# Kernel optimization log

Hardware: AMD Instinct MI355X
Metric: run time of the kernel (lower is better)

The kernel has to match this reference:

```python
import jax, jax.numpy as jnp
import numpy as np

Q_MAX = 127.0  # 8-bit, narrow range [-127, 127] (pytorch-quantization default)


def fake_quant(x, amax):
    """Fake quantization with clipped-STE semantics (matches pytorch-quantization).

    amax may be a scalar (per-tensor) or broadcastable (per-channel). Treated as
    a constant (stop_gradient'd by caller where appropriate).
    """
    amax = jnp.maximum(amax, 1e-12)
    scale = amax / Q_MAX
    xq = jnp.round(jnp.clip(x / scale, -Q_MAX, Q_MAX)) * scale
    xc = jnp.clip(x, -amax, amax)  # identity grad inside range, zero outside
    return xc + jax.lax.stop_gradient(xq - xc)


def quant_conv1x1(x, w, b):
    """QuantConv2d with 1x1 kernel: fake-quant input (per-tensor dynamic max amax)
    and weight (per-output-channel max amax), then conv + bias.
    x: [B,C,H,W], w: [O,C], b: [O]
    """
    a_amax = jax.lax.stop_gradient(jnp.max(jnp.abs(x)))
    xq = fake_quant(x, a_amax)
    w_amax = jax.lax.stop_gradient(jnp.max(jnp.abs(w), axis=1, keepdims=True))
    wq = fake_quant(w, w_amax)
    y = jnp.einsum('bchw,oc->bohw', xq, wq)
    return y + b[None, :, None, None]


def setup_inputs() -> dict:
    key = jax.random.key(0)
    k1, k2, k3, k4 = jax.random.split(key, 4)
    B, C, Cr, H, W = 64, 32, 8, 128, 128
    x = jax.random.normal(k1, (B, C, H, W), dtype=jnp.float32)
    identity = jax.random.normal(k2, (B, C, H, W), dtype=jnp.float32)
    w_reduce = jax.random.normal(k3, (Cr, C), dtype=jnp.float32) * 0.1
    b_reduce = jnp.zeros((Cr,), dtype=jnp.float32)
    w_expand = jax.random.normal(k4, (C, Cr), dtype=jnp.float32) * 0.1
    b_expand = jnp.zeros((C,), dtype=jnp.float32)
    return {"x": x, "identity": identity,
            "w_reduce": w_reduce, "b_reduce": b_reduce,
            "w_expand": w_expand, "b_expand": b_expand}


def reference(x, identity, w_reduce, b_reduce, w_expand, b_expand):
    h = quant_conv1x1(x, w_reduce, b_reduce)      # [B,8,H,W]
    h = h * jax.nn.sigmoid(h)                     # SiLU
    g = quant_conv1x1(h, w_expand, b_expand)      # [B,32,H,W]
    return identity * jax.nn.sigmoid(g)
```

## Files before the change

kernel.cpp:

```cpp
#include <hip/hip_runtime.h>
#include <math.h>

#define QMAX 127.0f
#define CIN 32
#define CR 8
#define HW 16384
#define BATCH 64
#define NPIX (BATCH*HW)
#define NQUAD (NPIX/4)
#define NX (BATCH*CIN*HW)

#define H_OFF 64
#define WS_NEEDED ((size_t)(H_OFF + (size_t)NPIX * CR) * 4)

__device__ __forceinline__ float fq(float v, float inv_scale, float scale) {
    return rintf(fminf(fmaxf(v * inv_scale, -QMAX), QMAX)) * scale;
}
__device__ __forceinline__ float sigmoidf_(float v) {
    return 1.0f / (1.0f + __expf(-v));
}

__global__ __launch_bounds__(256) void k1_xmax(const float4* __restrict__ x4,
                                               unsigned int* __restrict__ wsu) {
    int idx = blockIdx.x * 256 + threadIdx.x;
    float m = 0.f;
#pragma unroll
    for (int i = 0; i < 16; i++) {
        float4 v = x4[idx + i * 524288];
        m = fmaxf(m, fmaxf(fmaxf(fabsf(v.x), fabsf(v.y)), fmaxf(fabsf(v.z), fabsf(v.w))));
    }
#pragma unroll
    for (int off = 32; off > 0; off >>= 1) m = fmaxf(m, __shfl_xor(m, off, 64));
    __shared__ float red[4];
    int t = threadIdx.x;
    if ((t & 63) == 0) red[t >> 6] = m;
    __syncthreads();
    if (t == 0) {
        m = fmaxf(fmaxf(red[0], red[1]), fmaxf(red[2], red[3]));
        atomicMax(&wsu[0], __float_as_uint(m));
    }
}

__global__ __launch_bounds__(256) void k2_hmax(const float* __restrict__ x,
                                               const float* __restrict__ wr,
                                               const float* __restrict__ br,
                                               const unsigned int* __restrict__ wsu,
                                               unsigned int* __restrict__ hmax,
                                               float* __restrict__ hbuf) {
    __shared__ float wq[CR * CIN], bsh[CR], amr[CR];
    int t = threadIdx.x;
    if (t < CR) {
        float mm = 0.f;
        for (int c = 0; c < CIN; c++) mm = fmaxf(mm, fabsf(wr[t * CIN + c]));
        amr[t] = fmaxf(mm, 1e-12f);
        bsh[t] = br[t];
    }
    __syncthreads();
    {
        float amax = amr[t >> 5];
        wq[t] = fq(wr[t], QMAX / amax, amax * (1.f / QMAX));
    }
    __syncthreads();
    float a_amax = fmaxf(__uint_as_float(wsu[0]), 1e-12f);
    float scale = a_amax * (1.f / QMAX), inv_scale = QMAX / a_amax;
    int tid = blockIdx.x * 256 + t;
    int b = tid >> 12;
    int hw = (tid & 4095) << 2;
    const float* xb = x + (size_t)b * CIN * HW + hw;
    float hacc[CR][4];
#pragma unroll
    for (int o = 0; o < CR; o++)
#pragma unroll
        for (int v = 0; v < 4; v++) hacc[o][v] = 0.f;
#pragma unroll
    for (int c = 0; c < CIN; c++) {
        float4 xv = *(const float4*)(xb + (size_t)c * HW);
        float q0 = fq(xv.x, inv_scale, scale), q1 = fq(xv.y, inv_scale, scale);
        float q2 = fq(xv.z, inv_scale, scale), q3 = fq(xv.w, inv_scale, scale);
#pragma unroll
        for (int o = 0; o < CR; o++) {
            float w = wq[o * CIN + c];
            hacc[o][0] += q0 * w; hacc[o][1] += q1 * w;
            hacc[o][2] += q2 * w; hacc[o][3] += q3 * w;
        }
    }
    float m = 0.f;
#pragma unroll
    for (int o = 0; o < CR; o++) {
        float bb = bsh[o];
        float4 hv;
        float* hp = (float*)&hv;
#pragma unroll
        for (int v = 0; v < 4; v++) {
            float h = hacc[o][v] + bb;
            h = h * sigmoidf_(h);
            hp[v] = h;
            m = fmaxf(m, fabsf(h));
        }
        if (hbuf) *(float4*)(hbuf + ((size_t)(b * CR + o)) * HW + hw) = hv;
    }
#pragma unroll
    for (int off = 32; off > 0; off >>= 1) m = fmaxf(m, __shfl_xor(m, off, 64));
    __shared__ float red[4];
    if ((t & 63) == 0) red[t >> 6] = m;
    __syncthreads();
    if (t == 0) {
        m = fmaxf(fmaxf(red[0], red[1]), fmaxf(red[2], red[3]));
        atomicMax(hmax, __float_as_uint(m));
    }
}

__global__ __launch_bounds__(256) void k3_out(const float* __restrict__ hbuf,
                                              const float* __restrict__ identity,
                                              const float* __restrict__ we,
                                              const float* __restrict__ be,
                                              const unsigned int* __restrict__ wsu,
                                              float* __restrict__ out) {
    const int y = blockIdx.y;
    __shared__ float wqe[16 * CR], besh[16], ame[16];
    int t = threadIdx.x;
    if (t < 16) {
        int r = 16 * y + t;
        float mm = 0.f;
        for (int c = 0; c < CR; c++) mm = fmaxf(mm, fabsf(we[r * CR + c]));
        ame[t] = fmaxf(mm, 1e-12f);
        besh[t] = be[r];
    }
    __syncthreads();
    if (t < 128) {
        int r16 = t >> 3;
        float amax = ame[r16];
        wqe[t] = fq(we[(16 * y + r16) * CR + (t & 7)], QMAX / amax, amax * (1.f / QMAX));
    }
    __syncthreads();
    float h_amax = fmaxf(__uint_as_float(wsu[1]), 1e-12f);
    float hscale = h_amax * (1.f / QMAX), hinv = QMAX / h_amax;
    int tid = blockIdx.x * 256 + t;
    int b = tid >> 12;
    int hw = (tid & 4095) << 2;
    size_t base = (size_t)b * CIN * HW + hw;

    float hq[CR][4];
#pragma unroll
    for (int cr = 0; cr < CR; cr++) {
        float4 hv = *(const float4*)(hbuf + ((size_t)(b * CR + cr)) * HW + hw);
        hq[cr][0] = fq(hv.x, hinv, hscale);
        hq[cr][1] = fq(hv.y, hinv, hscale);
        hq[cr][2] = fq(hv.z, hinv, hscale);
        hq[cr][3] = fq(hv.w, hinv, hscale);
    }
#pragma unroll 4
    for (int o = 0; o < 16; o++) {
        float g0 = besh[o], g1 = g0, g2 = g0, g3 = g0;
#pragma unroll
        for (int cr = 0; cr < CR; cr++) {
            float w = wqe[o * CR + cr];
            g0 += hq[cr][0] * w; g1 += hq[cr][1] * w;
            g2 += hq[cr][2] * w; g3 += hq[cr][3] * w;
        }
        size_t off = base + (size_t)(16 * y + o) * HW;
        float4 idv = *(const float4*)(identity + off);
        float4 ov;
        ov.x = idv.x * sigmoidf_(g0);
        ov.y = idv.y * sigmoidf_(g1);
        ov.z = idv.z * sigmoidf_(g2);
        ov.w = idv.w * sigmoidf_(g3);
        *(float4*)(out + off) = ov;
    }
}

__global__ __launch_bounds__(256) void k3_out_rc(const float* __restrict__ x,
                                                 const float* __restrict__ identity,
                                                 const float* __restrict__ wr,
                                                 const float* __restrict__ br,
                                                 const float* __restrict__ we,
                                                 const float* __restrict__ be,
                                                 const unsigned int* __restrict__ wsu,
                                                 float* __restrict__ out) {
    __shared__ float wqr[CR * CIN], wqe[CIN * CR], bsh[CR], besh[CIN], amr[CR], ame[CIN];
    int t = threadIdx.x;
    if (t < CR) {
        float mm = 0.f;
        for (int c = 0; c < CIN; c++) mm = fmaxf(mm, fabsf(wr[t * CIN + c]));
        amr[t] = fmaxf(mm, 1e-12f);
        bsh[t] = br[t];
    }
    if (t >= 64 && t < 64 + CIN) {
        int r = t - 64;
        float mm = 0.f;
        for (int c = 0; c < CR; c++) mm = fmaxf(mm, fabsf(we[r * CR + c]));
        ame[r] = fmaxf(mm, 1e-12f);
        besh[r] = be[r];
    }
    __syncthreads();
    {
        float amax = amr[t >> 5];
        wqr[t] = fq(wr[t], QMAX / amax, amax * (1.f / QMAX));
        float amax2 = ame[t >> 3];
        wqe[t] = fq(we[t], QMAX / amax2, amax2 * (1.f / QMAX));
    }
    __syncthreads();
    float a_amax = fmaxf(__uint_as_float(wsu[0]), 1e-12f);
    float ascale = a_amax * (1.f / QMAX), ainv = QMAX / a_amax;
    float h_amax = fmaxf(__uint_as_float(wsu[1]), 1e-12f);
    float hscale = h_amax * (1.f / QMAX), hinv = QMAX / h_amax;
    int tid = blockIdx.x * 256 + t;
    int b = tid >> 12;
    int hw = (tid & 4095) << 2;
    size_t base = (size_t)b * CIN * HW + hw;
    const float* xb = x + base;
    float hq[CR][4];
    {
        float hacc[CR][4];
#pragma unroll
        for (int o = 0; o < CR; o++)
#pragma unroll
            for (int v = 0; v < 4; v++) hacc[o][v] = 0.f;
#pragma unroll
        for (int c = 0; c < CIN; c++) {
            float4 xv = *(const float4*)(xb + (size_t)c * HW);
            float q0 = fq(xv.x, ainv, ascale), q1 = fq(xv.y, ainv, ascale);
            float q2 = fq(xv.z, ainv, ascale), q3 = fq(xv.w, ainv, ascale);
#pragma unroll
            for (int o = 0; o < CR; o++) {
                float w = wqr[o * CIN + c];
                hacc[o][0] += q0 * w; hacc[o][1] += q1 * w;
                hacc[o][2] += q2 * w; hacc[o][3] += q3 * w;
            }
        }
#pragma unroll
        for (int o = 0; o < CR; o++) {
            float bb = bsh[o];
#pragma unroll
            for (int v = 0; v < 4; v++) {
                float h = hacc[o][v] + bb;
                h = h * sigmoidf_(h);
                hq[o][v] = fq(h, hinv, hscale);
            }
        }
    }
#pragma unroll 4
    for (int o2 = 0; o2 < CIN; o2++) {
        float g0 = besh[o2], g1 = g0, g2 = g0, g3 = g0;
#pragma unroll
        for (int cr = 0; cr < CR; cr++) {
            float w = wqe[o2 * CR + cr];
            g0 += hq[cr][0] * w; g1 += hq[cr][1] * w;
            g2 += hq[cr][2] * w; g3 += hq[cr][3] * w;
        }
        size_t off = base + (size_t)o2 * HW;
        float4 idv = *(const float4*)(identity + off);
        float4 ov;
        ov.x = idv.x * sigmoidf_(g0);
        ov.y = idv.y * sigmoidf_(g1);
        ov.z = idv.z * sigmoidf_(g2);
        ov.w = idv.w * sigmoidf_(g3);
        *(float4*)(out + off) = ov;
    }
}

extern "C" void kernel_launch(void* const* d_in, const int* in_sizes, int n_in,
                              void* d_out, int out_size, void* d_ws, size_t ws_size,
                              hipStream_t stream) {
    const float* x        = (const float*)d_in[0];
    const float* identity = (const float*)d_in[1];
    const float* wr       = (const float*)d_in[2];
    const float* br       = (const float*)d_in[3];
    const float* we       = (const float*)d_in[4];
    const float* be       = (const float*)d_in[5];
    float* out            = (float*)d_out;
    float* wsf            = (float*)d_ws;
    unsigned int* wsu     = (unsigned int*)d_ws;
    const bool big_ws     = (ws_size >= WS_NEEDED);
    float* hbuf           = big_ws ? (wsf + H_OFF) : nullptr;

    hipMemsetAsync(d_ws, 0, 16, stream);
    hipLaunchKernelGGL(k1_xmax, dim3(2048), dim3(256), 0, stream, (const float4*)x, wsu);
    hipLaunchKernelGGL(k2_hmax, dim3(NQUAD / 256), dim3(256), 0, stream,
                       x, wr, br, wsu, &wsu[1], hbuf);
    if (big_ws) {
        hipLaunchKernelGGL(k3_out, dim3(NQUAD / 256, 2), dim3(256), 0, stream,
                           hbuf, identity, we, be, wsu, out);
    } else {
        hipLaunchKernelGGL(k3_out_rc, dim3(NQUAD / 256), dim3(256), 0, stream,
                           x, identity, wr, br, we, be, wsu, out);
    }
}
```

Measured before the change: 382.9 us.

## Fuse SE block into single cooperative kernel with grid-wide syncs

Adds a cooperative kernel that does three phases in one launch, separated by grid syncs: the input abs-max, the reduce conv with SiLU plus the h abs-max, then the expand conv with the sigmoid gating. The h activations stay in registers across the grid sync, so the hbuf write and re-read and two extra launches go away. It also swaps the sigmoid division for a hardware reciprocal. The cost is that x is read twice inside one kernel, occupancy is pinned at 4 blocks per CU so all 1024 blocks can be resident, and every block stalls at each grid barrier. The old multi-kernel path stays as a fallback if cooperative launch is not possible.

```diff
diff --git a/kernel.cpp b/kernel.cpp
--- a/kernel.cpp
+++ b/kernel.cpp
@@ -1,5 +1,8 @@
 #include <hip/hip_runtime.h>
+#include <hip/hip_cooperative_groups.h>
 #include <math.h>
+
+namespace cg = cooperative_groups;
 
 #define QMAX 127.0f
 #define CIN 32
@@ -9,6 +12,7 @@
 #define NPIX (BATCH*HW)
 #define NQUAD (NPIX/4)
 #define NX (BATCH*CIN*HW)
+#define COOP_BLOCKS (NQUAD/256)
 
 #define H_OFF 64
 #define WS_NEEDED ((size_t)(H_OFF + (size_t)NPIX * CR) * 4)
@@ -17,7 +21,141 @@
     return rintf(fminf(fmaxf(v * inv_scale, -QMAX), QMAX)) * scale;
 }
 __device__ __forceinline__ float sigmoidf_(float v) {
-    return 1.0f / (1.0f + __expf(-v));
+    return __builtin_amdgcn_rcpf(1.0f + __expf(-v));
+}
+
+__global__ __launch_bounds__(256, 4) void se_fused(const float* __restrict__ x,
+                                                   const float* __restrict__ identity,
+                                                   const float* __restrict__ wr,
+                                                   const float* __restrict__ br,
+                                                   const float* __restrict__ we,
+                                                   const float* __restrict__ be,
+                                                   unsigned int* __restrict__ wsu,
+                                                   float* __restrict__ out) {
+    cg::grid_group grid = cg::this_grid();
+    int t = threadIdx.x;
+    __shared__ float wqr[CR * CIN], wqe[CIN * CR], bsh[CR], besh[CIN], amr[CR], ame[CIN];
+    __shared__ float red[4];
+
+    if (t < CR) {
+        float mm = 0.f;
+        for (int c = 0; c < CIN; c++) mm = fmaxf(mm, fabsf(wr[t * CIN + c]));
+        amr[t] = fmaxf(mm, 1e-12f);
+        bsh[t] = br[t];
+    }
+    if (t >= 64 && t < 64 + CIN) {
+        int r = t - 64;
+        float mm = 0.f;
+        for (int c = 0; c < CR; c++) mm = fmaxf(mm, fabsf(we[r * CR + c]));
+        ame[r] = fmaxf(mm, 1e-12f);
+        besh[r] = be[r];
+    }
+    __syncthreads();
+    {
+        float a1 = amr[t >> 5];
+        wqr[t] = fq(wr[t], QMAX / a1, a1 * (1.f / QMAX));
+        float a2 = ame[t >> 3];
+        wqe[t] = fq(we[t], QMAX / a2, a2 * (1.f / QMAX));
+    }
+    __syncthreads();
+
+    const int tid = blockIdx.x * 256 + t;
+
+    {
+        const float4* x4 = (const float4*)x;
+        float m = 0.f;
+#pragma unroll 8
+        for (int i = 0; i < 32; i++) {
+            float4 v = x4[tid + i * NQUAD];
+            m = fmaxf(m, fmaxf(fmaxf(fabsf(v.x), fabsf(v.y)), fmaxf(fabsf(v.z), fabsf(v.w))));
+        }
+#pragma unroll
+        for (int off = 32; off > 0; off >>= 1) m = fmaxf(m, __shfl_xor(m, off, 64));
+        if ((t & 63) == 0) red[t >> 6] = m;
+        __syncthreads();
+        if (t == 0) {
+            m = fmaxf(fmaxf(red[0], red[1]), fmaxf(red[2], red[3]));
+            atomicMax(&wsu[0], __float_as_uint(m));
+        }
+    }
+    grid.sync();
+
+    float a_amax = fmaxf(__uint_as_float(
+        __hip_atomic_load(&wsu[0], __ATOMIC_ACQUIRE, __HIP_MEMORY_SCOPE_AGENT)), 1e-12f);
+    float ascale = a_amax * (1.f / QMAX), ainv = QMAX / a_amax;
+    const int b = tid >> 12;
+    const int hw = (tid & 4095) << 2;
+    const size_t base = (size_t)b * CIN * HW + hw;
+    float h[CR][4];
+    {
+        float hacc[CR][4];
+#pragma unroll
+        for (int o = 0; o < CR; o++)
+#pragma unroll
+            for (int v = 0; v < 4; v++) hacc[o][v] = 0.f;
+        const float* xb = x + base;
+#pragma unroll
+        for (int c = 0; c < CIN; c++) {
+            float4 xv = *(const float4*)(xb + (size_t)c * HW);
+            float q0 = fq(xv.x, ainv, ascale), q1 = fq(xv.y, ainv, ascale);
+            float q2 = fq(xv.z, ainv, ascale), q3 = fq(xv.w, ainv, ascale);
+#pragma unroll
+            for (int o = 0; o < CR; o++) {
+                float w = wqr[o * CIN + c];
+                hacc[o][0] += q0 * w; hacc[o][1] += q1 * w;
+                hacc[o][2] += q2 * w; hacc[o][3] += q3 * w;
+            }
+        }
+        float m = 0.f;
+#pragma unroll
+        for (int o = 0; o < CR; o++) {
+            float bb = bsh[o];
+#pragma unroll
+            for (int v = 0; v < 4; v++) {
+                float hv = hacc[o][v] + bb;
+                hv = hv * sigmoidf_(hv);
+                h[o][v] = hv;
+                m = fmaxf(m, fabsf(hv));
+            }
+        }
+#pragma unroll
+        for (int off = 32; off > 0; off >>= 1) m = fmaxf(m, __shfl_xor(m, off, 64));
+        __syncthreads();
+        if ((t & 63) == 0) red[t >> 6] = m;
+        __syncthreads();
+        if (t == 0) {
+            m = fmaxf(fmaxf(red[0], red[1]), fmaxf(red[2], red[3]));
+            atomicMax(&wsu[1], __float_as_uint(m));
+        }
+    }
+    grid.sync();
+
+    float h_amax = fmaxf(__uint_as_float(
+        __hip_atomic_load(&wsu[1], __ATOMIC_ACQUIRE, __HIP_MEMORY_SCOPE_AGENT)), 1e-12f);
+    float hscale = h_amax * (1.f / QMAX), hinv = QMAX / h_amax;
+#pragma unroll
+    for (int o = 0; o < CR; o++)
+#pragma unroll
+        for (int v = 0; v < 4; v++) h[o][v] = fq(h[o][v], hinv, hscale);
+
+#pragma unroll 4
+    for (int o2 = 0; o2 < CIN; o2++) {
+        float g0 = besh[o2], g1 = g0, g2 = g0, g3 = g0;
+#pragma unroll
+        for (int cr = 0; cr < CR; cr++) {
+            float w = wqe[o2 * CR + cr];
+            g0 += h[cr][0] * w; g1 += h[cr][1] * w;
+            g2 += h[cr][2] * w; g3 += h[cr][3] * w;
+        }
+        size_t off = base + (size_t)o2 * HW;
+        float4 idv = *(const float4*)(identity + off);
+        float4 ov;
+        ov.x = idv.x * sigmoidf_(g0);
+        ov.y = idv.y * sigmoidf_(g1);
+        ov.z = idv.z * sigmoidf_(g2);
+        ov.w = idv.w * sigmoidf_(g3);
+        *(float4*)(out + off) = ov;
+    }
 }
 
 __global__ __launch_bounds__(256) void k1_xmax(const float4* __restrict__ x4,
@@ -139,7 +277,6 @@
     int b = tid >> 12;
     int hw = (tid & 4095) << 2;
     size_t base = (size_t)b * CIN * HW + hw;
-
     float hq[CR][4];
 #pragma unroll
     for (int cr = 0; cr < CR; cr++) {
@@ -271,10 +408,23 @@
     float* out            = (float*)d_out;
     float* wsf            = (float*)d_ws;
     unsigned int* wsu     = (unsigned int*)d_ws;
-    const bool big_ws     = (ws_size >= WS_NEEDED);
-    float* hbuf           = big_ws ? (wsf + H_OFF) : nullptr;
 
     hipMemsetAsync(d_ws, 0, 16, stream);
+
+    int maxb = 0;
+    hipError_t qerr = hipOccupancyMaxActiveBlocksPerMultiprocessor(&maxb, se_fused, 256, 0);
+    bool coop_ok = false;
+    if (qerr == hipSuccess && maxb >= 4) {
+        void* args[] = {(void*)&x, (void*)&identity, (void*)&wr, (void*)&br,
+                        (void*)&we, (void*)&be, (void*)&wsu, (void*)&out};
+        hipError_t lerr = hipLaunchCooperativeKernel((void*)se_fused, dim3(COOP_BLOCKS),
+                                                     dim3(256), args, 0, stream);
+        coop_ok = (lerr == hipSuccess);
+    }
+    if (coop_ok) return;
+
+    const bool big_ws = (ws_size >= WS_NEEDED);
+    float* hbuf = big_ws ? (wsf + H_OFF) : nullptr;
     hipLaunchKernelGGL(k1_xmax, dim3(2048), dim3(256), 0, stream, (const float4*)x, wsu);
     hipLaunchKernelGGL(k2_hmax, dim3(NQUAD / 256), dim3(256), 0, stream,
                        x, wr, br, wsu, &wsu[1], hbuf);
```

After: 375.0 us. -2.1%, faster.
